# Performance work log

Hardware: AMD Instinct MI355X
Metric: run time of the kernel (lower is better)

Reference implementation:

```python
import jax, jax.numpy as jnp
import numpy as np

# Production-scale dims: ViT patch attention on a 32x32 patch grid
B, L, F = 16, 1024, 512      # batch, seq (=NX*NY patches), model dim
H, D = 8, 64                 # heads, head_dim (F = H*D)
NX, NY = 32, 32              # patch grid; Toeplitz table size 4*NX*NY = 4096


def setup_inputs() -> dict:
    key = jax.random.key(0)
    ks = jax.random.split(key, 12)
    w = lambda k, shp: jax.random.normal(k, shp, jnp.float32) * 0.02
    return {
        "inputs_q": jax.random.normal(ks[0], (B, L, F), jnp.float32),
        "inputs_kv": jax.random.normal(ks[1], (B, L, F), jnp.float32),
        "Wq": w(ks[2], (F, H * D)), "bq": jnp.zeros((H * D,), jnp.float32),
        "Wk": w(ks[3], (F, H * D)), "bk": jnp.zeros((H * D,), jnp.float32),
        "Wv": w(ks[4], (F, H * D)), "bv": jnp.zeros((H * D,), jnp.float32),
        "Wo": w(ks[5], (H * D, F)), "bo": jnp.zeros((F,), jnp.float32),
        "toeplitz": w(ks[6], (H, 4 * NX * NY)),
    }


def _rel_index():
    # 2D relative-position (Toeplitz) index: patch p -> (x, y) on NX x NY grid.
    coords = jnp.arange(L)
    xi, yi = coords // NY, coords % NY
    dx = xi[:, None] - xi[None, :] + NX          # in [1, 2*NX-1]
    dy = yi[:, None] - yi[None, :] + NY          # in [1, 2*NY-1]
    return dx * (2 * NY) + dy                    # [L, L] indices into 4*NX*NY table


def reference(inputs_q, inputs_kv, Wq, bq, Wk, bk, Wv, bv, Wo, bo, toeplitz):
    q = (inputs_q @ Wq + bq).reshape(B, L, H, D)
    k = (inputs_kv @ Wk + bk).reshape(B, L, H, D)
    v = (inputs_kv @ Wv + bv).reshape(B, L, H, D)
    bias = toeplitz[:, _rel_index()]             # [H, L, L] Toeplitz relative bias
    scale = 1.0 / jnp.sqrt(jnp.float32(D))
    scores = jnp.einsum("bqhd,bkhd->bhqk", q, k) * scale + bias  # [B,H,L,L]
    attn = jax.nn.softmax(scores, axis=-1)
    x = jnp.einsum("bhqk,bkhd->bqhd", attn, v).reshape(B, L, H * D)
    out = x @ Wo + bo
    return out.reshape(B, L, H, D)               # matches torch forward's final reshape
```

## Files before the change

kernel.cpp:

```cpp
#include <hip/hip_runtime.h>
#include <hip/hip_bf16.h>

#define B_  16
#define L_  1024
#define F_  512
#define H_  8
#define D_  64
#define M_  (B_ * L_)
#define HD_ 512

typedef __bf16 bf16x8 __attribute__((ext_vector_type(8)));
typedef __bf16 bf16x4 __attribute__((ext_vector_type(4)));
typedef short  s16x4  __attribute__((ext_vector_type(4)));
typedef float  f32x4  __attribute__((ext_vector_type(4)));

__device__ __forceinline__ void gl_lds16(const void* g, void* l) {
  __builtin_amdgcn_global_load_lds(
      (const __attribute__((address_space(1))) unsigned int*)g,
      (__attribute__((address_space(3))) unsigned int*)l, 16, 0, 0);
}

__global__ __launch_bounds__(256) void wt_kernel(
    const float* __restrict__ Wq, const float* __restrict__ Wk,
    const float* __restrict__ Wv, const float* __restrict__ Wo,
    __bf16* __restrict__ Wt_all)
{
  const float* W = (blockIdx.z == 0) ? Wq : (blockIdx.z == 1) ? Wk
                 : (blockIdx.z == 2) ? Wv : Wo;
  __bf16* Wt = Wt_all + (size_t)blockIdx.z * (512 * 512);
  __shared__ float s[32][33];
  const int t = threadIdx.x;
  const int r = t >> 5, c = t & 31;
  const int k0 = blockIdx.x * 32, n0 = blockIdx.y * 32;
#pragma unroll
  for (int i = 0; i < 4; ++i)
    s[r + i * 8][c] = W[(size_t)(k0 + r + i * 8) * 512 + n0 + c];
  __syncthreads();
#pragma unroll
  for (int i = 0; i < 4; ++i)
    Wt[(size_t)(n0 + r + i * 8) * 512 + k0 + c] = (__bf16)s[c][r + i * 8];
}

__global__ __launch_bounds__(256) void gemm_proj_kernel(
    const float* __restrict__ Xq, const float* __restrict__ Xkv,
    const __bf16* __restrict__ Wt_all,
    const float* __restrict__ bq, const float* __restrict__ bk_,
    const float* __restrict__ bv_,
    __bf16* __restrict__ qd, __bf16* __restrict__ kd, __bf16* __restrict__ vd,
    int ybase)
{
  const int by = blockIdx.y + ybase;
  const int seg = by >> 2;
  const float* X = (seg == 0) ? Xq : Xkv;
  const __bf16* Wt = Wt_all + (size_t)seg * 262144;
  const float* bias = (seg == 0) ? bq : (seg == 1) ? bk_ : bv_;
  __bf16* dst = (seg == 0) ? qd : (seg == 1) ? kd : vd;
  const int mode = seg;

  __shared__ __align__(16) __bf16 As[2][4][128][8];
  __shared__ __align__(16) __bf16 Bs[2][4][128][8];
  const int t = threadIdx.x;
  const int m0 = blockIdx.x * 128, n0 = (by & 3) * 128;
  const int lane = t & 63, w = t >> 6;
  const int ml = lane & 15, quad = lane >> 4;
  const int wm = w & 1, wn = w >> 1;

  f32x4 acc[4][4];
#pragma unroll
  for (int i = 0; i < 4; ++i)
#pragma unroll
    for (int j = 0; j < 4; ++j) acc[i][j] = (f32x4){0.f, 0.f, 0.f, 0.f};

  const int ako0 = t & 3,          arow0 = t >> 2;
  const int ako1 = (t + 256) & 3,  arow1 = (t + 256) >> 2;
  const int bs0 = w * 64 + lane,   bs1 = (w + 4) * 64 + lane;
  const int bko0 = bs0 >> 7, brow0 = bs0 & 127;
  const int bko1 = bs1 >> 7, brow1 = bs1 & 127;

  float4 fa0, fa1, fa2, fa3;

#define ALOAD(kk)                                                               \
  do {                                                                          \
    const float* p0 = X + (size_t)(m0 + arow0) * 512 + (kk) + ako0 * 8;         \
    const float* p1 = X + (size_t)(m0 + arow1) * 512 + (kk) + ako1 * 8;         \
    fa0 = *(const float4*)p0; fa1 = *(const float4*)(p0 + 4);                   \
    fa2 = *(const float4*)p1; fa3 = *(const float4*)(p1 + 4);                   \
  } while (0)

#define AWRITE(buf)                                                             \
  do {                                                                          \
    bf16x8 v0, v1;                                                              \
    v0[0] = (__bf16)fa0.x; v0[1] = (__bf16)fa0.y; v0[2] = (__bf16)fa0.z;        \
    v0[3] = (__bf16)fa0.w; v0[4] = (__bf16)fa1.x; v0[5] = (__bf16)fa1.y;        \
    v0[6] = (__bf16)fa1.z; v0[7] = (__bf16)fa1.w;                               \
    v1[0] = (__bf16)fa2.x; v1[1] = (__bf16)fa2.y; v1[2] = (__bf16)fa2.z;        \
    v1[3] = (__bf16)fa2.w; v1[4] = (__bf16)fa3.x; v1[5] = (__bf16)fa3.y;        \
    v1[6] = (__bf16)fa3.z; v1[7] = (__bf16)fa3.w;                               \
    *(bf16x8*)&As[buf][ako0][arow0][0] = v0;                                    \
    *(bf16x8*)&As[buf][ako1][arow1][0] = v1;                                    \
  } while (0)

#define BSTAGE(buf, kk)                                                         \
  do {                                                                          \
    gl_lds16(&Wt[(size_t)(n0 + brow0) * 512 + (kk) + bko0 * 8],                 \
             &Bs[buf][bko0][brow0][0]);                                         \
    gl_lds16(&Wt[(size_t)(n0 + brow1) * 512 + (kk) + bko1 * 8],                 \
             &Bs[buf][bko1][brow1][0]);                                         \
  } while (0)

#define COMPUTE_TILE(buf)                                                       \
  do {                                                                          \
    bf16x8 a[4], b[4];                                                          \
    _Pragma("unroll") for (int mt = 0; mt < 4; ++mt)                            \
        a[mt] = *(const bf16x8*)&As[buf][quad][wm * 64 + mt * 16 + ml][0];      \
    _Pragma("unroll") for (int nt = 0; nt < 4; ++nt)                            \
        b[nt] = *(const bf16x8*)&Bs[buf][quad][wn * 64 + nt * 16 + ml][0];      \
    _Pragma("unroll") for (int mt = 0; mt < 4; ++mt)                            \
        _Pragma("unroll") for (int nt = 0; nt < 4; ++nt)                        \
            acc[mt][nt] = __builtin_amdgcn_mfma_f32_16x16x32_bf16(              \
                a[mt], b[nt], acc[mt][nt], 0, 0, 0);                            \
  } while (0)

  BSTAGE(0, 0);
  ALOAD(0);
  AWRITE(0);
  __syncthreads();

#pragma unroll
  for (int tt = 0; tt < 15; ++tt) {
    const int cur = tt & 1, nxt = cur ^ 1;
    ALOAD((tt + 1) * 32);
    BSTAGE(nxt, (tt + 1) * 32);
    COMPUTE_TILE(cur);
    AWRITE(nxt);
    __syncthreads();
  }
  COMPUTE_TILE(1);

#pragma unroll
  for (int nt = 0; nt < 4; ++nt) {
    int col = n0 + wn * 64 + nt * 16 + ml;
    float bv = bias[col];
    int h = col >> 6, d = col & 63;
#pragma unroll
    for (int mt = 0; mt < 4; ++mt) {
      int row0 = m0 + wm * 64 + mt * 16 + quad * 4;
      int bz = row0 >> 10;
      int l0 = row0 & 1023;
      if (mode == 2) {
        bf16x4 pk;
#pragma unroll
        for (int r = 0; r < 4; ++r) pk[r] = (__bf16)(acc[mt][nt][r] + bv);
        size_t idx = ((size_t)(bz * H_ + h) * D_ + d) * L_ + l0;
        *(bf16x4*)&dst[idx] = pk;
      } else {
        size_t base = ((size_t)(bz * H_ + h) * L_ + l0) * D_ + d;
#pragma unroll
        for (int r = 0; r < 4; ++r)
          dst[base + (size_t)r * D_] = (__bf16)(acc[mt][nt][r] + bv);
      }
    }
  }
#undef ALOAD
#undef AWRITE
#undef BSTAGE
#undef COMPUTE_TILE
}

__global__ __launch_bounds__(256, 2) void attn_kernel(
    const __bf16* __restrict__ qg,
    const __bf16* __restrict__ kg,
    const __bf16* __restrict__ vg,
    const float* __restrict__ toep_g,
    __bf16* __restrict__ xg)
{
  __shared__ float toep[4096];
  __shared__ __align__(16) __bf16 Ks[2][64][64];
  __shared__ __align__(16) __bf16 Vs[2][64][64];

  const int t = threadIdx.x;
  const int n = blockIdx.x;
  const int bh = ((n >> 5) << 3) | (n & 7);
  const int q0 = ((n >> 3) & 3) * 256;
  const int h = bh & 7;
  const int lane = t & 63, w = t >> 6;
  const int ml = lane & 15, quad = lane >> 4;
  const int lo3 = lane >> 3;
  const int kop = lane & 7;

  const size_t qkbase = (size_t)bh * (L_ * D_);
  const size_t vbase  = (size_t)bh * (D_ * L_);

  {
    const float4* src = (const float4*)(toep_g + (size_t)h * 4096);
    float4* dl = (float4*)toep;
    for (int i = t; i < 1024; i += 256) dl[i] = src[i];
  }

#pragma unroll
  for (int i = 0; i < 2; ++i) {
    int row = (w * 2 + i) * 8 + lo3;
    int ko = kop ^ lo3;
    gl_lds16(&kg[qkbase + (size_t)row * D_ + ko * 8], &Ks[0][row][kop * 8]);
    gl_lds16(&vg[vbase + (size_t)row * L_ + ko * 8], &Vs[0][row][kop * 8]);
  }

  bf16x8 qf[4][2];
#pragma unroll
  for (int qn = 0; qn < 4; ++qn) {
    const __bf16* qp =
        qg + qkbase + (size_t)(q0 + w * 64 + qn * 16 + ml) * D_ + quad * 8;
    qf[qn][0] = *(const bf16x8*)qp;
    qf[qn][1] = *(const bf16x8*)(qp + 32);
  }

  float lpart[4] = {0.f, 0.f, 0.f, 0.f};
  f32x4 o[4][4];
#pragma unroll
  for (int qn = 0; qn < 4; ++qn)
#pragma unroll
    for (int dt = 0; dt < 4; ++dt) o[qn][dt] = (f32x4){0.f, 0.f, 0.f, 0.f};

  __syncthreads();

  int cur = 0;
  for (int k0 = 0; k0 < L_; k0 += 64) {
    if (k0 + 64 < L_) {
      int nb = cur ^ 1;
#pragma unroll
      for (int i = 0; i < 2; ++i) {
        int row = (w * 2 + i) * 8 + lo3;
        int ko = kop ^ lo3;
        gl_lds16(&kg[qkbase + (size_t)(k0 + 64 + row) * D_ + ko * 8],
                 &Ks[nb][row][kop * 8]);
        gl_lds16(&vg[vbase + (size_t)row * L_ + k0 + 64 + ko * 8],
                 &Vs[nb][row][kop * 8]);
      }
    }

    const int cb0 = (((q0 + w * 64) >> 5) - (k0 >> 5) + 31) * 64 +
                    (ml - quad * 4 + 16);
    float tc[3][3][4];
#pragma unroll
    for (int a = 0; a < 3; ++a)
#pragma unroll
      for (int b = 0; b < 3; ++b) {
        const int cb = cb0 + a * 64 + b * 16;
#pragma unroll
        for (int r = 0; r < 4; ++r) tc[a][b][r] = toep[cb - r];
      }

#pragma unroll
    for (int nt = 0; nt < 4; ++nt) {
      bf16x8 kf0 = *(const bf16x8*)&Ks[cur][nt * 16 + ml][(quad ^ (ml & 7)) * 8];
      bf16x8 kf1 =
          *(const bf16x8*)&Ks[cur][nt * 16 + ml][((4 + quad) ^ (ml & 7)) * 8];

      s16x4 pfrag[4];
#pragma unroll
      for (int qn = 0; qn < 4; ++qn) {
        f32x4 z = (f32x4){0.f, 0.f, 0.f, 0.f};
        z = __builtin_amdgcn_mfma_f32_16x16x32_bf16(kf0, qf[qn][0], z, 0, 0, 0);
        z = __builtin_amdgcn_mfma_f32_16x16x32_bf16(kf1, qf[qn][1], z, 0, 0, 0);

        float p[4];
#pragma unroll
        for (int r = 0; r < 4; ++r)
          p[r] = __expf(fmaf(z[r], 0.125f,
                             tc[(qn >> 1) - (nt >> 1) + 1]
                               [(qn & 1) - (nt & 1) + 1][r]));
        lpart[qn] += (p[0] + p[1]) + (p[2] + p[3]);
        bf16x4 pk;
#pragma unroll
        for (int r = 0; r < 4; ++r) pk[r] = (__bf16)p[r];
        pfrag[qn] = __builtin_bit_cast(s16x4, pk);
      }

#pragma unroll
      for (int dt = 0; dt < 4; ++dt) {
        int row = dt * 16 + ml;
        int gc = nt * 2 + (quad >> 1);
        bf16x4 vfr = *(const bf16x4*)
            &Vs[cur][row][((gc ^ (row & 7)) * 8) + (quad & 1) * 4];
        s16x4 vfs = __builtin_bit_cast(s16x4, vfr);
#pragma unroll
        for (int qn = 0; qn < 4; ++qn)
          o[qn][dt] = __builtin_amdgcn_mfma_f32_16x16x16bf16_1k(
              pfrag[qn], vfs, o[qn][dt], 0, 0, 0);
      }
    }

    __syncthreads();
    cur ^= 1;
  }

#pragma unroll
  for (int qn = 0; qn < 4; ++qn) {
    lpart[qn] += __shfl_xor(lpart[qn], 16);
    lpart[qn] += __shfl_xor(lpart[qn], 32);
  }
  float linv[4][4];
#pragma unroll
  for (int qn = 0; qn < 4; ++qn)
#pragma unroll
    for (int r = 0; r < 4; ++r)
      linv[qn][r] = 1.0f / __shfl(lpart[qn], quad * 16 + quad * 4 + r);

#pragma unroll
  for (int qn = 0; qn < 4; ++qn)
#pragma unroll
    for (int dt = 0; dt < 4; ++dt)
#pragma unroll
      for (int r = 0; r < 4; ++r) {
        int row = q0 + w * 64 + qn * 16 + quad * 4 + r;
        xg[((size_t)(bh >> 3) * L_ + row) * 512 + h * 64 + dt * 16 + ml] =
            (__bf16)(o[qn][dt][r] * linv[qn][r]);
      }
}

__global__ __launch_bounds__(256, 4) void gemm_out_kernel(
    const __bf16* __restrict__ Xb,
    const __bf16* __restrict__ Wt,
    const float* __restrict__ bo,
    float* __restrict__ out)
{
  __shared__ __align__(16) __bf16 As[2][4][128][8];
  __shared__ __align__(16) __bf16 Bs[2][4][128][8];
  const int t = threadIdx.x;
  const int m0 = blockIdx.x * 128, n0 = blockIdx.y * 128;
  const int lane = t & 63, w = t >> 6;
  const int ml = lane & 15, quad = lane >> 4;
  const int wm = w & 1, wn = w >> 1;

  f32x4 acc[4][4];
#pragma unroll
  for (int i = 0; i < 4; ++i)
#pragma unroll
    for (int j = 0; j < 4; ++j) acc[i][j] = (f32x4){0.f, 0.f, 0.f, 0.f};

  const int slot0 = w * 64 + lane;
  const int slot1 = (w + 4) * 64 + lane;
  const int ko0 = slot0 >> 7, row0_ = slot0 & 127;
  const int ko1 = slot1 >> 7, row1_ = slot1 & 127;

#define STAGE_OUT(buf, kk)                                                      \
  do {                                                                          \
    gl_lds16(&Xb[(size_t)(m0 + row0_) * 512 + (kk) + ko0 * 8],                  \
             &As[buf][ko0][row0_][0]);                                          \
    gl_lds16(&Wt[(size_t)(n0 + row0_) * 512 + (kk) + ko0 * 8],                  \
             &Bs[buf][ko0][row0_][0]);                                          \
    gl_lds16(&Xb[(size_t)(m0 + row1_) * 512 + (kk) + ko1 * 8],                  \
             &As[buf][ko1][row1_][0]);                                          \
    gl_lds16(&Wt[(size_t)(n0 + row1_) * 512 + (kk) + ko1 * 8],                  \
             &Bs[buf][ko1][row1_][0]);                                          \
  } while (0)

#define COMPUTE_TILE_O(buf)                                                     \
  do {                                                                          \
    bf16x8 a[4], b[4];                                                          \
    _Pragma("unroll") for (int mt = 0; mt < 4; ++mt)                            \
        a[mt] = *(const bf16x8*)&As[buf][quad][wm * 64 + mt * 16 + ml][0];      \
    _Pragma("unroll") for (int nt = 0; nt < 4; ++nt)                            \
        b[nt] = *(const bf16x8*)&Bs[buf][quad][wn * 64 + nt * 16 + ml][0];      \
    _Pragma("unroll") for (int mt = 0; mt < 4; ++mt)                            \
        _Pragma("unroll") for (int nt = 0; nt < 4; ++nt)                        \
            acc[mt][nt] = __builtin_amdgcn_mfma_f32_16x16x32_bf16(              \
                a[mt], b[nt], acc[mt][nt], 0, 0, 0);                            \
  } while (0)

  STAGE_OUT(0, 0);
#pragma unroll
  for (int tt = 0; tt < 15; ++tt) {
    const int cur = tt & 1;
    STAGE_OUT(cur ^ 1, (tt + 1) * 32);
    asm volatile("s_waitcnt vmcnt(4)" ::: "memory");
    asm volatile("s_barrier" ::: "memory");
    COMPUTE_TILE_O(cur);
    asm volatile("s_barrier" ::: "memory");
  }
  asm volatile("s_waitcnt vmcnt(0)" ::: "memory");
  asm volatile("s_barrier" ::: "memory");
  COMPUTE_TILE_O(1);

#pragma unroll
  for (int nt = 0; nt < 4; ++nt) {
    int col = n0 + wn * 64 + nt * 16 + ml;
    float bv = bo[col];
#pragma unroll
    for (int mt = 0; mt < 4; ++mt) {
      int row0 = m0 + wm * 64 + mt * 16 + quad * 4;
#pragma unroll
      for (int r = 0; r < 4; ++r)
        out[(size_t)(row0 + r) * 512 + col] = acc[mt][nt][r] + bv;
    }
  }
#undef STAGE_OUT
#undef COMPUTE_TILE_O
}

extern "C" void kernel_launch(void* const* d_in, const int* in_sizes, int n_in,
                              void* d_out, int out_size, void* d_ws, size_t ws_size,
                              hipStream_t stream) {
  const float* inputs_q  = (const float*)d_in[0];
  const float* inputs_kv = (const float*)d_in[1];
  const float* Wq = (const float*)d_in[2];
  const float* bq = (const float*)d_in[3];
  const float* Wk = (const float*)d_in[4];
  const float* bk = (const float*)d_in[5];
  const float* Wv = (const float*)d_in[6];
  const float* bv = (const float*)d_in[7];
  const float* Wo = (const float*)d_in[8];
  const float* bo = (const float*)d_in[9];
  const float* toep = (const float*)d_in[10];
  float* out = (float*)d_out;

  char* ws = (char*)d_ws;
  __bf16* qb  = (__bf16*)(ws);
  __bf16* kb  = (__bf16*)(ws + 16777216);
  __bf16* vb  = (__bf16*)(ws + 33554432);
  __bf16* xb  = (__bf16*)(ws + 50331648);
  __bf16* Wt  = (__bf16*)(ws + 67108864);

  wt_kernel<<<dim3(16, 16, 4), 256, 0, stream>>>(Wq, Wk, Wv, Wo, Wt);
  gemm_proj_kernel<<<dim3(128, 6), 256, 0, stream>>>(
      inputs_q, inputs_kv, Wt, bq, bk, bv, qb, kb, vb, 0);
  gemm_proj_kernel<<<dim3(128, 6), 256, 0, stream>>>(
      inputs_q, inputs_kv, Wt, bq, bk, bv, qb, kb, vb, 6);
  attn_kernel<<<dim3(512), 256, 0, stream>>>(qb, kb, vb, toep, xb);
  gemm_out_kernel<<<dim3(128, 4), 256, 0, stream>>>(xb, Wt + 3 * 262144, bo, out);
}
```

Before: 262.4 us.

## Triple-buffer LDS staging across projection, attention and output GEMM kernels

Switches the projection GEMM, attention and output GEMM kernels from double- to triple-buffered async global-to-LDS staging, prefetching two tiles ahead. Each loop iteration now needs one barrier instead of two, with explicit vmcnt waits. The attention kernel also pre-scales the Toeplitz table by log2(e) and uses exp2f with a folded scale constant, saving a multiply per exponent. The extra LDS buffers raise shared memory per block, and the output GEMM's launch bound drops from 4 to 2 blocks per CU, which can reduce occupancy.

```diff
diff --git a/kernel.cpp b/kernel.cpp
--- a/kernel.cpp
+++ b/kernel.cpp
@@ -19,6 +19,10 @@
       (const __attribute__((address_space(1))) unsigned int*)g,
       (__attribute__((address_space(3))) unsigned int*)l, 16, 0, 0);
 }
+
+#define WAIT_VM_LG(N)                                                           \
+  asm volatile("s_waitcnt vmcnt(" #N ") lgkmcnt(0)" ::: "memory")
+#define BARRIER() asm volatile("s_barrier" ::: "memory")
 
 __global__ __launch_bounds__(256) void wt_kernel(
     const float* __restrict__ Wq, const float* __restrict__ Wk,
@@ -58,7 +62,7 @@
   const int mode = seg;
 
   __shared__ __align__(16) __bf16 As[2][4][128][8];
-  __shared__ __align__(16) __bf16 Bs[2][4][128][8];
+  __shared__ __align__(16) __bf16 Bs[3][4][128][8];
   const int t = threadIdx.x;
   const int m0 = blockIdx.x * 128, n0 = (by & 3) * 128;
   const int lane = t & 63, w = t >> 6;
@@ -108,7 +112,263 @@
              &Bs[buf][bko1][brow1][0]);                                         \
   } while (0)
 
-#define COMPUTE_TILE(buf)                                                       \
+#define COMPUTE_TILE(ab, bb)                                                    \
+  do {                                                                          \
+    bf16x8 a[4], b[4];                                                          \
+    _Pragma("unroll") for (int mt = 0; mt < 4; ++mt)                            \
+        a[mt] = *(const bf16x8*)&As[ab][quad][wm * 64 + mt * 16 + ml][0];       \
+    _Pragma("unroll") for (int nt = 0; nt < 4; ++nt)                            \
+        b[nt] = *(const bf16x8*)&Bs[bb][quad][wn * 64 + nt * 16 + ml][0];       \
+    _Pragma("unroll") for (int mt = 0; mt < 4; ++mt)                            \
+        _Pragma("unroll") for (int nt = 0; nt < 4; ++nt)                        \
+            acc[mt][nt] = __builtin_amdgcn_mfma_f32_16x16x32_bf16(              \
+                a[mt], b[nt], acc[mt][nt], 0, 0, 0);                            \
+  } while (0)
+
+  ALOAD(0);
+  BSTAGE(0, 0);
+  BSTAGE(1, 32);
+  AWRITE(0);
+  WAIT_VM_LG(2);
+  BARRIER();
+
+  int bcur = 0, bst = 2;
+  for (int tt = 0; tt < 16; ++tt) {
+    if (tt < 15) ALOAD((tt + 1) * 32);
+    if (tt < 14) BSTAGE(bst, (tt + 2) * 32);
+    COMPUTE_TILE(tt & 1, bcur);
+    if (tt < 14) {
+      WAIT_VM_LG(2);
+      AWRITE((tt + 1) & 1);
+      asm volatile("s_waitcnt lgkmcnt(0)" ::: "memory");
+      BARRIER();
+    } else if (tt == 14) {
+      WAIT_VM_LG(0);
+      AWRITE((tt + 1) & 1);
+      asm volatile("s_waitcnt lgkmcnt(0)" ::: "memory");
+      BARRIER();
+    }
+    bcur = (bcur == 2) ? 0 : bcur + 1;
+    bst = (bst == 2) ? 0 : bst + 1;
+  }
+
+#pragma unroll
+  for (int nt = 0; nt < 4; ++nt) {
+    int col = n0 + wn * 64 + nt * 16 + ml;
+    float bv = bias[col];
+    int h = col >> 6, d = col & 63;
+#pragma unroll
+    for (int mt = 0; mt < 4; ++mt) {
+      int row0 = m0 + wm * 64 + mt * 16 + quad * 4;
+      int bz = row0 >> 10;
+      int l0 = row0 & 1023;
+      if (mode == 2) {
+        bf16x4 pk;
+#pragma unroll
+        for (int r = 0; r < 4; ++r) pk[r] = (__bf16)(acc[mt][nt][r] + bv);
+        size_t idx = ((size_t)(bz * H_ + h) * D_ + d) * L_ + l0;
+        *(bf16x4*)&dst[idx] = pk;
+      } else {
+        size_t base = ((size_t)(bz * H_ + h) * L_ + l0) * D_ + d;
+#pragma unroll
+        for (int r = 0; r < 4; ++r)
+          dst[base + (size_t)r * D_] = (__bf16)(acc[mt][nt][r] + bv);
+      }
+    }
+  }
+#undef ALOAD
+#undef AWRITE
+#undef BSTAGE
+#undef COMPUTE_TILE
+}
+
+__global__ __launch_bounds__(256, 2) void attn_kernel(
+    const __bf16* __restrict__ qg,
+    const __bf16* __restrict__ kg,
+    const __bf16* __restrict__ vg,
+    const float* __restrict__ toep_g,
+    __bf16* __restrict__ xg)
+{
+  __shared__ float toep[4096];
+  __shared__ __align__(16) __bf16 Ks[3][64][64];
+  __shared__ __align__(16) __bf16 Vs[3][64][64];
+
+  const int t = threadIdx.x;
+  const int n = blockIdx.x;
+  const int bh = ((n >> 5) << 3) | (n & 7);
+  const int q0 = ((n >> 3) & 3) * 256;
+  const int h = bh & 7;
+  const int lane = t & 63, w = t >> 6;
+  const int ml = lane & 15, quad = lane >> 4;
+  const int lo3 = lane >> 3;
+  const int kop = lane & 7;
+
+  const size_t qkbase = (size_t)bh * (L_ * D_);
+  const size_t vbase  = (size_t)bh * (D_ * L_);
+
+  {
+    const float4* src = (const float4*)(toep_g + (size_t)h * 4096);
+    float4* dl = (float4*)toep;
+    for (int i = t; i < 1024; i += 256) {
+      float4 v = src[i];
+      v.x *= 1.44269504f; v.y *= 1.44269504f;
+      v.z *= 1.44269504f; v.w *= 1.44269504f;
+      dl[i] = v;
+    }
+  }
+
+#define KV_STAGE(buf, k0n)                                                      \
+  do {                                                                          \
+    _Pragma("unroll") for (int i = 0; i < 2; ++i) {                             \
+      int row = (w * 2 + i) * 8 + lo3;                                          \
+      int ko = kop ^ lo3;                                                       \
+      gl_lds16(&kg[qkbase + (size_t)((k0n) + row) * D_ + ko * 8],               \
+               &Ks[buf][row][kop * 8]);                                         \
+      gl_lds16(&vg[vbase + (size_t)row * L_ + (k0n) + ko * 8],                  \
+               &Vs[buf][row][kop * 8]);                                         \
+    }                                                                           \
+  } while (0)
+
+  KV_STAGE(0, 0);
+  KV_STAGE(1, 64);
+
+  bf16x8 qf[4][2];
+#pragma unroll
+  for (int qn = 0; qn < 4; ++qn) {
+    const __bf16* qp =
+        qg + qkbase + (size_t)(q0 + w * 64 + qn * 16 + ml) * D_ + quad * 8;
+    qf[qn][0] = *(const bf16x8*)qp;
+    qf[qn][1] = *(const bf16x8*)(qp + 32);
+  }
+
+  float lpart[4] = {0.f, 0.f, 0.f, 0.f};
+  f32x4 o[4][4];
+#pragma unroll
+  for (int qn = 0; qn < 4; ++qn)
+#pragma unroll
+    for (int dt = 0; dt < 4; ++dt) o[qn][dt] = (f32x4){0.f, 0.f, 0.f, 0.f};
+
+#define ATTN_TILE(KB, K0)                                                       \
+  do {                                                                          \
+    const int cb0 = (((q0 + w * 64) >> 5) - ((K0) >> 5) + 31) * 64 +            \
+                    (ml - quad * 4 + 16);                                       \
+    float tc[3][3][4];                                                          \
+    _Pragma("unroll") for (int a = 0; a < 3; ++a)                               \
+      _Pragma("unroll") for (int b = 0; b < 3; ++b) {                           \
+        const int cb = cb0 + a * 64 + b * 16;                                   \
+        _Pragma("unroll") for (int r = 0; r < 4; ++r)                           \
+          tc[a][b][r] = toep[cb - r];                                           \
+      }                                                                         \
+    _Pragma("unroll") for (int nt = 0; nt < 4; ++nt) {                          \
+      bf16x8 kf0 =                                                              \
+          *(const bf16x8*)&Ks[KB][nt * 16 + ml][(quad ^ (ml & 7)) * 8];         \
+      bf16x8 kf1 =                                                              \
+          *(const bf16x8*)&Ks[KB][nt * 16 + ml][((4 + quad) ^ (ml & 7)) * 8];   \
+      s16x4 pfrag[4];                                                           \
+      _Pragma("unroll") for (int qn = 0; qn < 4; ++qn) {                        \
+        f32x4 z = (f32x4){0.f, 0.f, 0.f, 0.f};                                  \
+        z = __builtin_amdgcn_mfma_f32_16x16x32_bf16(kf0, qf[qn][0], z, 0,0,0);  \
+        z = __builtin_amdgcn_mfma_f32_16x16x32_bf16(kf1, qf[qn][1], z, 0,0,0);  \
+        float p[4];                                                             \
+        _Pragma("unroll") for (int r = 0; r < 4; ++r)                           \
+          p[r] = exp2f(fmaf(z[r], 0.18033688f,                                  \
+                            tc[(qn >> 1) - (nt >> 1) + 1]                       \
+                              [(qn & 1) - (nt & 1) + 1][r]));                   \
+        lpart[qn] += (p[0] + p[1]) + (p[2] + p[3]);                             \
+        bf16x4 pk;                                                              \
+        _Pragma("unroll") for (int r = 0; r < 4; ++r) pk[r] = (__bf16)p[r];     \
+        pfrag[qn] = __builtin_bit_cast(s16x4, pk);                              \
+      }                                                                         \
+      _Pragma("unroll") for (int dt = 0; dt < 4; ++dt) {                        \
+        int row = dt * 16 + ml;                                                 \
+        int gc = nt * 2 + (quad >> 1);                                          \
+        bf16x4 vfr = *(const bf16x4*)                                           \
+            &Vs[KB][row][((gc ^ (row & 7)) * 8) + (quad & 1) * 4];              \
+        s16x4 vfs = __builtin_bit_cast(s16x4, vfr);                             \
+        _Pragma("unroll") for (int qn = 0; qn < 4; ++qn)                        \
+          o[qn][dt] = __builtin_amdgcn_mfma_f32_16x16x16bf16_1k(                \
+              pfrag[qn], vfs, o[qn][dt], 0, 0, 0);                              \
+      }                                                                         \
+    }                                                                           \
+  } while (0)
+
+  int bcur = 0, bst = 2;
+  for (int tt = 0; tt < 15; ++tt) {
+    WAIT_VM_LG(4);
+    BARRIER();
+    if (tt < 14) KV_STAGE(bst, (tt + 2) << 6);
+    ATTN_TILE(bcur, tt << 6);
+    bcur = (bcur == 2) ? 0 : bcur + 1;
+    bst = (bst == 2) ? 0 : bst + 1;
+  }
+  WAIT_VM_LG(0);
+  BARRIER();
+  ATTN_TILE(bcur, 15 << 6);
+#undef ATTN_TILE
+#undef KV_STAGE
+
+#pragma unroll
+  for (int qn = 0; qn < 4; ++qn) {
+    lpart[qn] += __shfl_xor(lpart[qn], 16);
+    lpart[qn] += __shfl_xor(lpart[qn], 32);
+  }
+  float linv[4][4];
+#pragma unroll
+  for (int qn = 0; qn < 4; ++qn)
+#pragma unroll
+    for (int r = 0; r < 4; ++r)
+      linv[qn][r] = 1.0f / __shfl(lpart[qn], quad * 16 + quad * 4 + r);
+
+#pragma unroll
+  for (int qn = 0; qn < 4; ++qn)
+#pragma unroll
+    for (int dt = 0; dt < 4; ++dt)
+#pragma unroll
+      for (int r = 0; r < 4; ++r) {
+        int row = q0 + w * 64 + qn * 16 + quad * 4 + r;
+        xg[((size_t)(bh >> 3) * L_ + row) * 512 + h * 64 + dt * 16 + ml] =
+            (__bf16)(o[qn][dt][r] * linv[qn][r]);
+      }
+}
+
+__global__ __launch_bounds__(256, 2) void gemm_out_kernel(
+    const __bf16* __restrict__ Xb,
+    const __bf16* __restrict__ Wt,
+    const float* __restrict__ bo,
+    float* __restrict__ out)
+{
+  __shared__ __align__(16) __bf16 As[3][4][128][8];
+  __shared__ __align__(16) __bf16 Bs[3][4][128][8];
+  const int t = threadIdx.x;
+  const int m0 = blockIdx.x * 128, n0 = blockIdx.y * 128;
+  const int lane = t & 63, w = t >> 6;
+  const int ml = lane & 15, quad = lane >> 4;
+  const int wm = w & 1, wn = w >> 1;
+
+  f32x4 acc[4][4];
+#pragma unroll
+  for (int i = 0; i < 4; ++i)
+#pragma unroll
+    for (int j = 0; j < 4; ++j) acc[i][j] = (f32x4){0.f, 0.f, 0.f, 0.f};
+
+  const int slot0 = w * 64 + lane;
+  const int slot1 = (w + 4) * 64 + lane;
+  const int ko0 = slot0 >> 7, row0_ = slot0 & 127;
+  const int ko1 = slot1 >> 7, row1_ = slot1 & 127;
+
+#define STAGE_OUT(buf, kk)                                                      \
+  do {                                                                          \
+    gl_lds16(&Xb[(size_t)(m0 + row0_) * 512 + (kk) + ko0 * 8],                  \
+             &As[buf][ko0][row0_][0]);                                          \
+    gl_lds16(&Wt[(size_t)(n0 + row0_) * 512 + (kk) + ko0 * 8],                  \
+             &Bs[buf][ko0][row0_][0]);                                          \
+    gl_lds16(&Xb[(size_t)(m0 + row1_) * 512 + (kk) + ko1 * 8],                  \
+             &As[buf][ko1][row1_][0]);                                          \
+    gl_lds16(&Wt[(size_t)(n0 + row1_) * 512 + (kk) + ko1 * 8],                  \
+             &Bs[buf][ko1][row1_][0]);                                          \
+  } while (0)
+
+#define COMPUTE_TILE_O(buf)                                                     \
   do {                                                                          \
     bf16x8 a[4], b[4];                                                          \
     _Pragma("unroll") for (int mt = 0; mt < 4; ++mt)                            \
@@ -121,266 +381,21 @@
                 a[mt], b[nt], acc[mt][nt], 0, 0, 0);                            \
   } while (0)
 
-  BSTAGE(0, 0);
-  ALOAD(0);
-  AWRITE(0);
-  __syncthreads();
-
-#pragma unroll
+  STAGE_OUT(0, 0);
+  STAGE_OUT(1, 32);
+
+  int bcur = 0, bst = 2;
   for (int tt = 0; tt < 15; ++tt) {
-    const int cur = tt & 1, nxt = cur ^ 1;
-    ALOAD((tt + 1) * 32);
-    BSTAGE(nxt, (tt + 1) * 32);
-    COMPUTE_TILE(cur);
-    AWRITE(nxt);
-    __syncthreads();
-  }
-  COMPUTE_TILE(1);
-
-#pragma unroll
-  for (int nt = 0; nt < 4; ++nt) {
-    int col = n0 + wn * 64 + nt * 16 + ml;
-    float bv = bias[col];
-    int h = col >> 6, d = col & 63;
-#pragma unroll
-    for (int mt = 0; mt < 4; ++mt) {
-      int row0 = m0 + wm * 64 + mt * 16 + quad * 4;
-      int bz = row0 >> 10;
-      int l0 = row0 & 1023;
-      if (mode == 2) {
-        bf16x4 pk;
-#pragma unroll
-        for (int r = 0; r < 4; ++r) pk[r] = (__bf16)(acc[mt][nt][r] + bv);
-        size_t idx = ((size_t)(bz * H_ + h) * D_ + d) * L_ + l0;
-        *(bf16x4*)&dst[idx] = pk;
-      } else {
-        size_t base = ((size_t)(bz * H_ + h) * L_ + l0) * D_ + d;
-#pragma unroll
-        for (int r = 0; r < 4; ++r)
-          dst[base + (size_t)r * D_] = (__bf16)(acc[mt][nt][r] + bv);
-      }
-    }
-  }
-#undef ALOAD
-#undef AWRITE
-#undef BSTAGE
-#undef COMPUTE_TILE
-}
-
-__global__ __launch_bounds__(256, 2) void attn_kernel(
-    const __bf16* __restrict__ qg,
-    const __bf16* __restrict__ kg,
-    const __bf16* __restrict__ vg,
-    const float* __restrict__ toep_g,
-    __bf16* __restrict__ xg)
-{
-  __shared__ float toep[4096];
-  __shared__ __align__(16) __bf16 Ks[2][64][64];
-  __shared__ __align__(16) __bf16 Vs[2][64][64];
-
-  const int t = threadIdx.x;
-  const int n = blockIdx.x;
-  const int bh = ((n >> 5) << 3) | (n & 7);
-  const int q0 = ((n >> 3) & 3) * 256;
-  const int h = bh & 7;
-  const int lane = t & 63, w = t >> 6;
-  const int ml = lane & 15, quad = lane >> 4;
-  const int lo3 = lane >> 3;
-  const int kop = lane & 7;
-
-  const size_t qkbase = (size_t)bh * (L_ * D_);
-  const size_t vbase  = (size_t)bh * (D_ * L_);
-
-  {
-    const float4* src = (const float4*)(toep_g + (size_t)h * 4096);
-    float4* dl = (float4*)toep;
-    for (int i = t; i < 1024; i += 256) dl[i] = src[i];
-  }
-
-#pragma unroll
-  for (int i = 0; i < 2; ++i) {
-    int row = (w * 2 + i) * 8 + lo3;
-    int ko = kop ^ lo3;
-    gl_lds16(&kg[qkbase + (size_t)row * D_ + ko * 8], &Ks[0][row][kop * 8]);
-    gl_lds16(&vg[vbase + (size_t)row * L_ + ko * 8], &Vs[0][row][kop * 8]);
-  }
-
-  bf16x8 qf[4][2];
-#pragma unroll
-  for (int qn = 0; qn < 4; ++qn) {
-    const __bf16* qp =
-        qg + qkbase + (size_t)(q0 + w * 64 + qn * 16 + ml) * D_ + quad * 8;
-    qf[qn][0] = *(const bf16x8*)qp;
-    qf[qn][1] = *(const bf16x8*)(qp + 32);
-  }
-
-  float lpart[4] = {0.f, 0.f, 0.f, 0.f};
-  f32x4 o[4][4];
-#pragma unroll
-  for (int qn = 0; qn < 4; ++qn)
-#pragma unroll
-    for (int dt = 0; dt < 4; ++dt) o[qn][dt] = (f32x4){0.f, 0.f, 0.f, 0.f};
-
-  __syncthreads();
-
-  int cur = 0;
-  for (int k0 = 0; k0 < L_; k0 += 64) {
-    if (k0 + 64 < L_) {
-      int nb = cur ^ 1;
-#pragma unroll
-      for (int i = 0; i < 2; ++i) {
-        int row = (w * 2 + i) * 8 + lo3;
-        int ko = kop ^ lo3;
-        gl_lds16(&kg[qkbase + (size_t)(k0 + 64 + row) * D_ + ko * 8],
-                 &Ks[nb][row][kop * 8]);
-        gl_lds16(&vg[vbase + (size_t)row * L_ + k0 + 64 + ko * 8],
-                 &Vs[nb][row][kop * 8]);
-      }
-    }
-
-    const int cb0 = (((q0 + w * 64) >> 5) - (k0 >> 5) + 31) * 64 +
-                    (ml - quad * 4 + 16);
-    float tc[3][3][4];
-#pragma unroll
-    for (int a = 0; a < 3; ++a)
-#pragma unroll
-      for (int b = 0; b < 3; ++b) {
-        const int cb = cb0 + a * 64 + b * 16;
-#pragma unroll
-        for (int r = 0; r < 4; ++r) tc[a][b][r] = toep[cb - r];
-      }
-
-#pragma unroll
-    for (int nt = 0; nt < 4; ++nt) {
-      bf16x8 kf0 = *(const bf16x8*)&Ks[cur][nt * 16 + ml][(quad ^ (ml & 7)) * 8];
-      bf16x8 kf1 =
-          *(const bf16x8*)&Ks[cur][nt * 16 + ml][((4 + quad) ^ (ml & 7)) * 8];
-
-      s16x4 pfrag[4];
-#pragma unroll
-      for (int qn = 0; qn < 4; ++qn) {
-        f32x4 z = (f32x4){0.f, 0.f, 0.f, 0.f};
-        z = __builtin_amdgcn_mfma_f32_16x16x32_bf16(kf0, qf[qn][0], z, 0, 0, 0);
-        z = __builtin_amdgcn_mfma_f32_16x16x32_bf16(kf1, qf[qn][1], z, 0, 0, 0);
-
-        float p[4];
-#pragma unroll
-        for (int r = 0; r < 4; ++r)
-          p[r] = __expf(fmaf(z[r], 0.125f,
-                             tc[(qn >> 1) - (nt >> 1) + 1]
-                               [(qn & 1) - (nt & 1) + 1][r]));
-        lpart[qn] += (p[0] + p[1]) + (p[2] + p[3]);
-        bf16x4 pk;
-#pragma unroll
-        for (int r = 0; r < 4; ++r) pk[r] = (__bf16)p[r];
-        pfrag[qn] = __builtin_bit_cast(s16x4, pk);
-      }
-
-#pragma unroll
-      for (int dt = 0; dt < 4; ++dt) {
-        int row = dt * 16 + ml;
-        int gc = nt * 2 + (quad >> 1);
-        bf16x4 vfr = *(const bf16x4*)
-            &Vs[cur][row][((gc ^ (row & 7)) * 8) + (quad & 1) * 4];
-        s16x4 vfs = __builtin_bit_cast(s16x4, vfr);
-#pragma unroll
-        for (int qn = 0; qn < 4; ++qn)
-          o[qn][dt] = __builtin_amdgcn_mfma_f32_16x16x16bf16_1k(
-              pfrag[qn], vfs, o[qn][dt], 0, 0, 0);
-      }
-    }
-
-    __syncthreads();
-    cur ^= 1;
-  }
-
-#pragma unroll
-  for (int qn = 0; qn < 4; ++qn) {
-    lpart[qn] += __shfl_xor(lpart[qn], 16);
-    lpart[qn] += __shfl_xor(lpart[qn], 32);
-  }
-  float linv[4][4];
-#pragma unroll
-  for (int qn = 0; qn < 4; ++qn)
-#pragma unroll
-    for (int r = 0; r < 4; ++r)
-      linv[qn][r] = 1.0f / __shfl(lpart[qn], quad * 16 + quad * 4 + r);
-
-#pragma unroll
-  for (int qn = 0; qn < 4; ++qn)
-#pragma unroll
-    for (int dt = 0; dt < 4; ++dt)
-#pragma unroll
-      for (int r = 0; r < 4; ++r) {
-        int row = q0 + w * 64 + qn * 16 + quad * 4 + r;
-        xg[((size_t)(bh >> 3) * L_ + row) * 512 + h * 64 + dt * 16 + ml] =
-            (__bf16)(o[qn][dt][r] * linv[qn][r]);
-      }
-}
-
-__global__ __launch_bounds__(256, 4) void gemm_out_kernel(
-    const __bf16* __restrict__ Xb,
-    const __bf16* __restrict__ Wt,
-    const float* __restrict__ bo,
-    float* __restrict__ out)
-{
-  __shared__ __align__(16) __bf16 As[2][4][128][8];
-  __shared__ __align__(16) __bf16 Bs[2][4][128][8];
-  const int t = threadIdx.x;
-  const int m0 = blockIdx.x * 128, n0 = blockIdx.y * 128;
-  const int lane = t & 63, w = t >> 6;
-  const int ml = lane & 15, quad = lane >> 4;
-  const int wm = w & 1, wn = w >> 1;
-
-  f32x4 acc[4][4];
-#pragma unroll
-  for (int i = 0; i < 4; ++i)
-#pragma unroll
-    for (int j = 0; j < 4; ++j) acc[i][j] = (f32x4){0.f, 0.f, 0.f, 0.f};
-
-  const int slot0 = w * 64 + lane;
-  const int slot1 = (w + 4) * 64 + lane;
-  const int ko0 = slot0 >> 7, row0_ = slot0 & 127;
-  const int ko1 = slot1 >> 7, row1_ = slot1 & 127;
-
-#define STAGE_OUT(buf, kk)                                                      \
-  do {                                                                          \
-    gl_lds16(&Xb[(size_t)(m0 + row0_) * 512 + (kk) + ko0 * 8],                  \
-             &As[buf][ko0][row0_][0]);                                          \
-    gl_lds16(&Wt[(size_t)(n0 + row0_) * 512 + (kk) + ko0 * 8],                  \
-             &Bs[buf][ko0][row0_][0]);                                          \
-    gl_lds16(&Xb[(size_t)(m0 + row1_) * 512 + (kk) + ko1 * 8],                  \
-             &As[buf][ko1][row1_][0]);                                          \
-    gl_lds16(&Wt[(size_t)(n0 + row1_) * 512 + (kk) + ko1 * 8],                  \
-             &Bs[buf][ko1][row1_][0]);                                          \
-  } while (0)
-
-#define COMPUTE_TILE_O(buf)                                                     \
-  do {                                                                          \
-    bf16x8 a[4], b[4];                                                          \
-    _Pragma("unroll") for (int mt = 0; mt < 4; ++mt)                            \
-        a[mt] = *(const bf16x8*)&As[buf][quad][wm * 64 + mt * 16 + ml][0];      \
-    _Pragma("unroll") for (int nt = 0; nt < 4; ++nt)                            \
-        b[nt] = *(const bf16x8*)&Bs[buf][quad][wn * 64 + nt * 16 + ml][0];      \
-    _Pragma("unroll") for (int mt = 0; mt < 4; ++mt)                            \
-        _Pragma("unroll") for (int nt = 0; nt < 4; ++nt)                        \
-            acc[mt][nt] = __builtin_amdgcn_mfma_f32_16x16x32_bf16(              \
-                a[mt], b[nt], acc[mt][nt], 0, 0, 0);                            \
-  } while (0)
-
-  STAGE_OUT(0, 0);
-#pragma unroll
-  for (int tt = 0; tt < 15; ++tt) {
-    const int cur = tt & 1;
-    STAGE_OUT(cur ^ 1, (tt + 1) * 32);
-    asm volatile("s_waitcnt vmcnt(4)" ::: "memory");
-    asm volatile("s_barrier" ::: "memory");
-    COMPUTE_TILE_O(cur);
-    asm volatile("s_barrier" ::: "memory");
-  }
-  asm volatile("s_waitcnt vmcnt(0)" ::: "memory");
-  asm volatile("s_barrier" ::: "memory");
-  COMPUTE_TILE_O(1);
+    WAIT_VM_LG(4);
+    BARRIER();
+    if (tt < 14) STAGE_OUT(bst, (tt + 2) * 32);
+    COMPUTE_TILE_O(bcur);
+    bcur = (bcur == 2) ? 0 : bcur + 1;
+    bst = (bst == 2) ? 0 : bst + 1;
+  }
+  WAIT_VM_LG(0);
+  BARRIER();
+  COMPUTE_TILE_O(bcur);
 
 #pragma unroll
   for (int nt = 0; nt < 4; ++nt) {
```

Measured after the change: 272.6 us. 1.04x slower.
